# Kernel tuning notes

Measured on AMD Instinct MI355X. Metric: run time of the kernel, lower is better.

The kernel has to match this reference:

```python
import jax, jax.numpy as jnp
import numpy as np

N = 50000      # nodes
E = 1600000    # edges (avg degree 32)
D_IN = 128
HID = 64


def setup_inputs() -> dict:
    key = jax.random.key(0)
    ks = jax.random.split(key, 7)
    x = jax.random.normal(ks[0], (N, D_IN), dtype=jnp.float32)
    ei = jax.random.randint(ks[1], (2, E), 0, N, dtype=jnp.int32)
    ew = jax.random.uniform(ks[2], (E,), dtype=jnp.float32)
    # GCNConv linear weights (glorot-ish scale); lin has no bias, conv bias added post-aggregation
    W1 = jax.random.normal(ks[3], (HID, D_IN), dtype=jnp.float32) * (1.0 / np.sqrt(D_IN))
    b1 = jnp.zeros((HID,), dtype=jnp.float32)
    W2 = jax.random.normal(ks[4], (HID, HID), dtype=jnp.float32) * (1.0 / np.sqrt(HID))
    b2 = jnp.zeros((HID,), dtype=jnp.float32)
    return {"x": x, "ei": ei, "ew": ew, "W1": W1, "b1": b1, "W2": W2, "b2": b2}


def _gcn_conv(x, src, dst, ew_all, W, b, n_nodes):
    """PyG GCNConv: gcn_norm (self-loops already appended) + x@W.T, gather-scale-scatter, +b."""
    deg = jax.ops.segment_sum(ew_all, dst, num_segments=n_nodes)  # dst-side weighted degree
    dinv = jnp.where(deg > 0, jax.lax.rsqrt(deg), 0.0)            # deg^{-1/2}, inf->0
    norm = dinv[src] * ew_all * dinv[dst]                          # [E+N]
    h = x @ W.T                                                    # [N, hid]
    msg = h[src] * norm[:, None]                                   # gather + scale
    out = jax.ops.segment_sum(msg, dst, num_segments=n_nodes)     # scatter-add
    return out + b


def reference(x, ei, ew, W1, b1, W2, b2):
    n_nodes = x.shape[0]
    # add self loops once (fill value 1.0), shared by both conv layers
    loop = jnp.arange(n_nodes, dtype=ei.dtype)
    src = jnp.concatenate([ei[0], loop])
    dst = jnp.concatenate([ei[1], loop])
    ew_all = jnp.concatenate([ew, jnp.ones((n_nodes,), dtype=ew.dtype)])

    h1 = jax.nn.relu(_gcn_conv(x, src, dst, ew_all, W1, b1, n_nodes))
    # dropout is identity in eval mode
    h2 = _gcn_conv(h1, src, dst, ew_all, W2, b2, n_nodes)
    return h2 + h1
```

## Files before the change

kernel.cpp:

```cpp
#include <hip/hip_runtime.h>

#define HID 64
#define DIN 128
#define NBLK 512
#define CSH 14
#define CAP (1 << CSH)
#define PAD 68

typedef unsigned long long ull;
typedef unsigned short u16;

static __device__ __forceinline__ u16 f2bf(float f) {
  unsigned u = __float_as_uint(f);
  unsigned lsb = (u >> 16) & 1u;
  u += 0x7fffu + lsb;
  return (u16)(u >> 16);
}


template <int K, int NT, bool XT_PRELOADED>
__device__ __forceinline__ void gemm_tile(const float* __restrict__ X,
                                          const float* __restrict__ W,
                                          u16* __restrict__ out,
                                          float* XT, float* WL,
                                          int n0, int n_nodes, int tid) {
  constexpr int ROWS = NT / 8;
  const int tx = tid & 15;
  const int ty = tid >> 4;
  float acc[2][4] = {{0.f}};

  for (int ph = 0; ph < K / 64; ++ph) {
    const int d0 = ph * 64;
    __syncthreads();
    if (!XT_PRELOADED) {
#pragma unroll
      for (int k = 0; k < 2; ++k) {
        int f = tid + k * NT;
        int r = f >> 4, q = f & 15;
        int n = n0 + r;
        float4 xv = (n < n_nodes)
          ? *reinterpret_cast<const float4*>(&X[(size_t)n * K + d0 + 4 * q])
          : make_float4(0.f, 0.f, 0.f, 0.f);
        *reinterpret_cast<float4*>(&XT[r * PAD + 4 * q]) = xv;
      }
    }
#pragma unroll
    for (int k = 0; k < 1024 / NT; ++k) {
      int gq = tid + k * NT;
      int qd = gq >> 6, j = gq & 63;
      float4 wv = *reinterpret_cast<const float4*>(&W[(size_t)j * K + d0 + 4 * qd]);
      WL[(4 * qd + 0) * PAD + j] = wv.x;
      WL[(4 * qd + 1) * PAD + j] = wv.y;
      WL[(4 * qd + 2) * PAD + j] = wv.z;
      WL[(4 * qd + 3) * PAD + j] = wv.w;
    }
    __syncthreads();
#pragma unroll 4
    for (int dd = 0; dd < 64; dd += 4) {
      float4 ws[4];
#pragma unroll
      for (int dk = 0; dk < 4; ++dk)
        ws[dk] = *reinterpret_cast<const float4*>(&WL[(dd + dk) * PAD + 4 * tx]);
      float4 x0 = *reinterpret_cast<const float4*>(&XT[ty * PAD + dd]);
      float4 x1 = *reinterpret_cast<const float4*>(&XT[(ty + ROWS / 2) * PAD + dd]);
      float xm0[4] = {x0.x, x0.y, x0.z, x0.w};
      float xm1[4] = {x1.x, x1.y, x1.z, x1.w};
#pragma unroll
      for (int dk = 0; dk < 4; ++dk) {
        acc[0][0] = fmaf(xm0[dk], ws[dk].x, acc[0][0]);
        acc[0][1] = fmaf(xm0[dk], ws[dk].y, acc[0][1]);
        acc[0][2] = fmaf(xm0[dk], ws[dk].z, acc[0][2]);
        acc[0][3] = fmaf(xm0[dk], ws[dk].w, acc[0][3]);
        acc[1][0] = fmaf(xm1[dk], ws[dk].x, acc[1][0]);
        acc[1][1] = fmaf(xm1[dk], ws[dk].y, acc[1][1]);
        acc[1][2] = fmaf(xm1[dk], ws[dk].z, acc[1][2]);
        acc[1][3] = fmaf(xm1[dk], ws[dk].w, acc[1][3]);
      }
    }
  }

#pragma unroll
  for (int mi = 0; mi < 2; ++mi) {
    int n = n0 + mi * (ROWS / 2) + ty;
    if (n < n_nodes) {
      ushort4 o = make_ushort4(f2bf(acc[mi][0]), f2bf(acc[mi][1]),
                               f2bf(acc[mi][2]), f2bf(acc[mi][3]));
      *reinterpret_cast<ushort4*>(&out[(size_t)n * HID + 4 * tx]) = o;
    }
  }
}


__global__ __launch_bounds__(512) void k_build_gemm(const int* __restrict__ src,
                                                    const int* __restrict__ dst,
                                                    const float* __restrict__ ew,
                                                    int* __restrict__ cursor,
                                                    int2* __restrict__ bufA,
                                                    int E, int chunk,
                                                    const float* __restrict__ x,
                                                    const float* __restrict__ W1,
                                                    u16* __restrict__ h,
                                                    int n_nodes) {
  __shared__ float S[2 * 64 * PAD];
  int b = blockIdx.x, tid = threadIdx.x;
  if (b >= NBLK) {
    gemm_tile<DIN, 512, false>(x, W1, h, S, S + 64 * PAD, (b - NBLK) * 64, n_nodes, tid);
    return;
  }
  int* hst = (int*)S;
  int* cur = (int*)S + 256;
  if (tid < 256) hst[tid] = 0;
  __syncthreads();
  int e0 = b * chunk, e1 = min(E, e0 + chunk);
  int nfull = (e1 - e0) & ~3;
  int rtail = (e1 - e0) - nfull;
  for (int e = e0 + 4 * tid; e < e0 + nfull; e += 4 * 512) {
    int4 d4 = *reinterpret_cast<const int4*>(&dst[e]);
    atomicAdd(&hst[d4.x >> 8], 1);
    atomicAdd(&hst[d4.y >> 8], 1);
    atomicAdd(&hst[d4.z >> 8], 1);
    atomicAdd(&hst[d4.w >> 8], 1);
  }
  if (tid < rtail) atomicAdd(&hst[dst[e0 + nfull + tid] >> 8], 1);
  __syncthreads();
  if (tid < 256) {
    int c = hst[tid];
    int ofs = (c > 0) ? atomicAdd(&cursor[tid], c) : 0;
    cur[tid] = (tid << CSH) + ofs;
  }
  __syncthreads();
  for (int e = e0 + 4 * tid; e < e0 + nfull; e += 4 * 512) {
    int4 s4 = *reinterpret_cast<const int4*>(&src[e]);
    int4 d4 = *reinterpret_cast<const int4*>(&dst[e]);
    float4 w4 = *reinterpret_cast<const float4*>(&ew[e]);
    int p0 = atomicAdd(&cur[d4.x >> 8], 1);
    bufA[p0] = make_int2(__float_as_int(w4.x), (int)(((unsigned)s4.x << 16) | (unsigned)d4.x));
    int p1 = atomicAdd(&cur[d4.y >> 8], 1);
    bufA[p1] = make_int2(__float_as_int(w4.y), (int)(((unsigned)s4.y << 16) | (unsigned)d4.y));
    int p2 = atomicAdd(&cur[d4.z >> 8], 1);
    bufA[p2] = make_int2(__float_as_int(w4.z), (int)(((unsigned)s4.z << 16) | (unsigned)d4.z));
    int p3 = atomicAdd(&cur[d4.w >> 8], 1);
    bufA[p3] = make_int2(__float_as_int(w4.w), (int)(((unsigned)s4.w << 16) | (unsigned)d4.w));
  }
  if (tid < rtail) {
    int e = e0 + nfull + tid;
    int s = src[e], d = dst[e];
    int p = atomicAdd(&cur[d >> 8], 1);
    bufA[p] = make_int2(__float_as_int(ew[e]), (int)(((unsigned)s << 16) | (unsigned)d));
  }
}


__global__ __launch_bounds__(1024) void k_passB(const int2* __restrict__ bufA,
                                                const int* __restrict__ cursor,
                                                int2* __restrict__ bufB,
                                                int* __restrict__ offs,
                                                int* __restrict__ cnt,
                                                float* __restrict__ dinv,
                                                int NBC, int N) {
  int bin = blockIdx.x, tid = threadIdx.x;
  __shared__ int h2[256];
  __shared__ int cur[256];
  __shared__ float dg[256];
  int bbase = bin << CSH;
  int m = cursor[bin];
  if (tid < 256) { h2[tid] = 0; dg[tid] = 0.f; }
  __syncthreads();
  int2 rloc[16];
#pragma unroll
  for (int k = 0; k < 16; ++k) {
    int i = tid + k * 1024;
    if (i < m) {
      rloc[k] = bufA[bbase + i];
      atomicAdd(&h2[(unsigned)rloc[k].y & 255u], 1);
    }
  }
  __syncthreads();
  int own = (tid < 256) ? h2[tid] : 0;
  for (int o = 1; o < 256; o <<= 1) {
    int u = 0;
    if (tid < 256 && tid >= o) u = h2[tid - o];
    __syncthreads();
    if (tid < 256) h2[tid] += u;
    __syncthreads();
  }
  int nd = (bin << 8) + tid;
  if (tid < 256) {
    int excl = h2[tid] - own;
    cur[tid] = excl;
    if (nd < N) { offs[nd] = bbase + excl; cnt[nd] = own; }
  }
  __syncthreads();
#pragma unroll
  for (int k = 0; k < 16; ++k) {
    int i = tid + k * 1024;
    if (i < m) {
      int2 r = rloc[k];
      unsigned sd = (unsigned)r.y;
      int dl = (int)(sd & 255u);
      int p = atomicAdd(&cur[dl], 1);
      bufB[bbase + p] = make_int2(r.x, (int)(sd >> 16));
      atomicAdd(&dg[dl], __int_as_float(r.x));
    }
  }
  __syncthreads();
  if (tid < 256 && nd < N) dinv[nd] = rsqrtf(1.0f + dg[tid]);
}


__device__ __forceinline__ void bfma8(const uint4& v, float w, float* a) {
  a[0] = fmaf(__uint_as_float(v.x << 16), w, a[0]);
  a[1] = fmaf(__uint_as_float(v.x & 0xffff0000u), w, a[1]);
  a[2] = fmaf(__uint_as_float(v.y << 16), w, a[2]);
  a[3] = fmaf(__uint_as_float(v.y & 0xffff0000u), w, a[3]);
  a[4] = fmaf(__uint_as_float(v.z << 16), w, a[4]);
  a[5] = fmaf(__uint_as_float(v.z & 0xffff0000u), w, a[5]);
  a[6] = fmaf(__uint_as_float(v.w << 16), w, a[6]);
  a[7] = fmaf(__uint_as_float(v.w & 0xffff0000u), w, a[7]);
}

__device__ __forceinline__ void agg_node(const u16* __restrict__ h,
                                         const int2* __restrict__ recs,
                                         const float* __restrict__ dinv,
                                         int beg, int end, int node, float di,
                                         int lane, int p8, float* r) {
  float a[8], b[8];
  {
    uint4 v = *reinterpret_cast<const uint4*>(&h[(size_t)node * HID + p8]);
    a[0] = __uint_as_float(v.x << 16) * di;
    a[1] = __uint_as_float(v.x & 0xffff0000u) * di;
    a[2] = __uint_as_float(v.y << 16) * di;
    a[3] = __uint_as_float(v.y & 0xffff0000u) * di;
    a[4] = __uint_as_float(v.z << 16) * di;
    a[5] = __uint_as_float(v.z & 0xffff0000u) * di;
    a[6] = __uint_as_float(v.w << 16) * di;
    a[7] = __uint_as_float(v.w & 0xffff0000u) * di;
#pragma unroll
    for (int j = 0; j < 8; ++j) b[j] = 0.f;
  }

  const int gb = lane & 56;
  const int l7 = lane & 7;
  int i = beg;
  if (i + 8 <= end) {
    ull rr = *reinterpret_cast<const ull*>(&recs[i + l7]);
    float dv = dinv[(int)(rr >> 32)];
    for (;;) {
      float wd = __uint_as_float((unsigned)rr) * dv;
      ull ru = (rr & 0xffffffff00000000ull) | (ull)__float_as_uint(wd);
      bool more = (i + 16 <= end);
      ull rr_n = 0; float dv_n = 0.f;
      if (more) {
        rr_n = *reinterpret_cast<const ull*>(&recs[i + 8 + l7]);
        dv_n = dinv[(int)(rr_n >> 32)];
      }
#pragma unroll
      for (int k = 0; k < 8; ++k) {
        ull q = __shfl(ru, gb | k, 64);
        float wk = __uint_as_float((unsigned)q);
        int sk = (int)(q >> 32);
        uint4 vk = *reinterpret_cast<const uint4*>(&h[(size_t)sk * HID + p8]);
        bfma8(vk, wk, (k & 1) ? b : a);
      }
      i += 8;
      if (!more) break;
      rr = rr_n; dv = dv_n;
    }
  }
  if (i + 4 <= end) {
    int2 r0 = recs[i];     int2 r1 = recs[i + 1];
    int2 r2 = recs[i + 2]; int2 r3 = recs[i + 3];
    uint4 v0 = *reinterpret_cast<const uint4*>(&h[(size_t)r0.y * HID + p8]);
    uint4 v1 = *reinterpret_cast<const uint4*>(&h[(size_t)r1.y * HID + p8]);
    uint4 v2 = *reinterpret_cast<const uint4*>(&h[(size_t)r2.y * HID + p8]);
    uint4 v3 = *reinterpret_cast<const uint4*>(&h[(size_t)r3.y * HID + p8]);
    bfma8(v0, __int_as_float(r0.x) * dinv[r0.y], a);
    bfma8(v1, __int_as_float(r1.x) * dinv[r1.y], b);
    bfma8(v2, __int_as_float(r2.x) * dinv[r2.y], a);
    bfma8(v3, __int_as_float(r3.x) * dinv[r3.y], b);
    i += 4;
  }
  if (i + 2 <= end) {
    int2 r0 = recs[i];     int2 r1 = recs[i + 1];
    uint4 v0 = *reinterpret_cast<const uint4*>(&h[(size_t)r0.y * HID + p8]);
    uint4 v1 = *reinterpret_cast<const uint4*>(&h[(size_t)r1.y * HID + p8]);
    bfma8(v0, __int_as_float(r0.x) * dinv[r0.y], a);
    bfma8(v1, __int_as_float(r1.x) * dinv[r1.y], b);
    i += 2;
  }
  if (i < end) {
    int2 r0 = recs[i];
    uint4 v0 = *reinterpret_cast<const uint4*>(&h[(size_t)r0.y * HID + p8]);
    bfma8(v0, __int_as_float(r0.x) * dinv[r0.y], a);
  }
#pragma unroll
  for (int j = 0; j < 8; ++j) r[j] = (a[j] + b[j]) * di;
}


__global__ __launch_bounds__(256) void k_agg_gemm(const u16* __restrict__ h,
                                                  const int2* __restrict__ recs,
                                                  const int* __restrict__ offs,
                                                  const int* __restrict__ cnt,
                                                  const float* __restrict__ dinv,
                                                  const float* __restrict__ bias,
                                                  const float* __restrict__ W2,
                                                  float* __restrict__ h1,
                                                  u16* __restrict__ h2,
                                                  int n_nodes) {
  __shared__ float S[(32 + 64) * PAD];
  float* XT = S;
  float* WL = S + 32 * PAD;
  int tid = threadIdx.x;
  int lane = tid & 63;
  int p8 = (lane & 7) * 8;
  int nl = (tid >> 6) * 8 + (lane >> 3);
  int node = blockIdx.x * 32 + nl;
  if (node < n_nodes) {
    float di = dinv[node];
    float r[8];
    agg_node(h, recs, dinv, offs[node], offs[node] + cnt[node], node, di,
             lane, p8, r);
    float4 bb0 = *reinterpret_cast<const float4*>(&bias[p8]);
    float4 bb1 = *reinterpret_cast<const float4*>(&bias[p8 + 4]);
    r[0] += bb0.x; r[1] += bb0.y; r[2] += bb0.z; r[3] += bb0.w;
    r[4] += bb1.x; r[5] += bb1.y; r[6] += bb1.z; r[7] += bb1.w;
#pragma unroll
    for (int j = 0; j < 8; ++j) r[j] = fmaxf(r[j], 0.f);
    float4 lo = make_float4(r[0], r[1], r[2], r[3]);
    float4 hi = make_float4(r[4], r[5], r[6], r[7]);
    *reinterpret_cast<float4*>(&h1[(size_t)node * HID + p8]) = lo;
    *reinterpret_cast<float4*>(&h1[(size_t)node * HID + p8 + 4]) = hi;
    *reinterpret_cast<float4*>(&XT[nl * PAD + p8]) = lo;
    *reinterpret_cast<float4*>(&XT[nl * PAD + p8 + 4]) = hi;
  }
  gemm_tile<HID, 256, true>(nullptr, W2, h2, XT, WL, blockIdx.x * 32, n_nodes, tid);
}


__global__ __launch_bounds__(256) void k_agg2(const u16* __restrict__ h,
                                              const int2* __restrict__ recs,
                                              const int* __restrict__ offs,
                                              const int* __restrict__ cnt,
                                              const float* __restrict__ dinv,
                                              const float* __restrict__ bias,
                                              const float* __restrict__ resid,
                                              float* __restrict__ out, int n_nodes) {
  int tid = threadIdx.x;
  int lane = tid & 63;
  int p8 = (lane & 7) * 8;
  int node = (blockIdx.x * 4 + (tid >> 6)) * 8 + (lane >> 3);
  if (node >= n_nodes) return;
  float di = dinv[node];
  float r[8];
  agg_node(h, recs, dinv, offs[node], offs[node] + cnt[node], node, di,
           lane, p8, r);
  float4 bb0 = *reinterpret_cast<const float4*>(&bias[p8]);
  float4 bb1 = *reinterpret_cast<const float4*>(&bias[p8 + 4]);
  float4 rs0 = *reinterpret_cast<const float4*>(&resid[(size_t)node * HID + p8]);
  float4 rs1 = *reinterpret_cast<const float4*>(&resid[(size_t)node * HID + p8 + 4]);
  r[0] += bb0.x + rs0.x; r[1] += bb0.y + rs0.y;
  r[2] += bb0.z + rs0.z; r[3] += bb0.w + rs0.w;
  r[4] += bb1.x + rs1.x; r[5] += bb1.y + rs1.y;
  r[6] += bb1.z + rs1.z; r[7] += bb1.w + rs1.w;
  *reinterpret_cast<float4*>(&out[(size_t)node * HID + p8]) =
      make_float4(r[0], r[1], r[2], r[3]);
  *reinterpret_cast<float4*>(&out[(size_t)node * HID + p8 + 4]) =
      make_float4(r[4], r[5], r[6], r[7]);
}


extern "C" void kernel_launch(void* const* d_in, const int* in_sizes, int n_in,
                              void* d_out, int out_size, void* d_ws, size_t ws_size,
                              hipStream_t stream) {
  const float* x  = (const float*)d_in[0];
  const int*   ei = (const int*)d_in[1];
  const float* ew = (const float*)d_in[2];
  const float* W1 = (const float*)d_in[3];
  const float* b1 = (const float*)d_in[4];
  const float* W2 = (const float*)d_in[5];
  const float* b2 = (const float*)d_in[6];
  float* out = (float*)d_out;

  const int N = in_sizes[0] / DIN;
  const int E = in_sizes[2];
  const int* src = ei;
  const int* dst = ei + E;

  const int NBC = (N + 255) >> 8;
  const int chunk = (((E + NBLK - 1) / NBLK) + 3) & ~3;
  const int nslab = NBC << CSH;

  char* p = (char*)d_ws;
  auto carve = [&](size_t bytes) {
    char* r = p;
    p += (bytes + 255) & ~(size_t)255;
    return r;
  };
  int*   cursor = (int*)carve(256 * 4);
  int*   offs   = (int*)carve((size_t)N * 4);
  int*   cnt    = (int*)carve((size_t)N * 4);
  float* dinv   = (float*)carve((size_t)N * 4);
  int2*  bufA   = (int2*)carve((size_t)nslab * 8);
  int2*  bufB   = (int2*)carve((size_t)nslab * 8);
  u16*   h      = (u16*)carve((size_t)N * HID * 2);
  u16*   h2     = (u16*)carve((size_t)N * HID * 2);
  float* h1     = (float*)carve((size_t)N * HID * 4);

  int gblk  = (N + 63) / 64;
  int gblk2 = (N + 31) / 32;
  int ablk  = (N + 31) / 32;

  hipMemsetAsync(cursor, 0, 256 * 4, stream);
  k_build_gemm<<<NBLK + gblk, 512, 0, stream>>>(src, dst, ew, cursor, bufA, E, chunk,
                                                x, W1, h, N);
  k_passB<<<NBC, 1024, 0, stream>>>(bufA, cursor, bufB, offs, cnt, dinv, NBC, N);
  k_agg_gemm<<<gblk2, 256, 0, stream>>>(h, bufB, offs, cnt, dinv, b1, W2, h1, h2, N);
  k_agg2<<<ablk, 256, 0, stream>>>(h2, bufB, offs, cnt, dinv, b2, h1, out, N);
}
```

Before: 209.5 us.

## Split bin histogram per half-block and keep first edge loads in registers

The edge-binning phase now keeps two shared-memory histograms and cursor arrays, one per 256-thread half of the block, to reduce contention on the LDS atomics. The src, dst and weight values for each thread's first two int4 groups are held in registers between the count pass and the scatter pass, so they are not read from global memory twice. Only edges beyond the first 4096 in a chunk are re-read. Scalar tail handling was removed, so correctness now depends on chunk boundaries being multiples of 4.

```diff
diff --git a/kernel.cpp b/kernel.cpp
--- a/kernel.cpp
+++ b/kernel.cpp
@@ -107,46 +107,77 @@
     gemm_tile<DIN, 512, false>(x, W1, h, S, S + 64 * PAD, (b - NBLK) * 64, n_nodes, tid);
     return;
   }
-  int* hst = (int*)S;
-  int* cur = (int*)S + 256;
-  if (tid < 256) hst[tid] = 0;
+  int* h0   = (int*)S;
+  int* h1_  = (int*)S + 256;
+  int* cur0 = (int*)S + 512;
+  int* cur1 = (int*)S + 768;
+  if (tid < 256) { h0[tid] = 0; h1_[tid] = 0; }
   __syncthreads();
   int e0 = b * chunk, e1 = min(E, e0 + chunk);
-  int nfull = (e1 - e0) & ~3;
-  int rtail = (e1 - e0) - nfull;
-  for (int e = e0 + 4 * tid; e < e0 + nfull; e += 4 * 512) {
-    int4 d4 = *reinterpret_cast<const int4*>(&dst[e]);
-    atomicAdd(&hst[d4.x >> 8], 1);
-    atomicAdd(&hst[d4.y >> 8], 1);
-    atomicAdd(&hst[d4.z >> 8], 1);
-    atomicAdd(&hst[d4.w >> 8], 1);
-  }
-  if (tid < rtail) atomicAdd(&hst[dst[e0 + nfull + tid] >> 8], 1);
+  const int half = tid >> 8;
+  int* hh = half ? h1_ : h0;
+  int4 s4[2], d4[2];
+  float4 w4[2];
+  bool val[2];
+#pragma unroll
+  for (int it = 0; it < 2; ++it) {
+    int e = e0 + 4 * tid + it * 2048;
+    val[it] = (e < e1);
+    if (val[it]) {
+      s4[it] = *reinterpret_cast<const int4*>(&src[e]);
+      d4[it] = *reinterpret_cast<const int4*>(&dst[e]);
+      w4[it] = *reinterpret_cast<const float4*>(&ew[e]);
+      atomicAdd(&hh[d4[it].x >> 8], 1);
+      atomicAdd(&hh[d4[it].y >> 8], 1);
+      atomicAdd(&hh[d4[it].z >> 8], 1);
+      atomicAdd(&hh[d4[it].w >> 8], 1);
+    }
+  }
+  for (int e = e0 + 4096 + 4 * tid; e < e1; e += 2048) {
+    int4 dd = *reinterpret_cast<const int4*>(&dst[e]);
+    atomicAdd(&hh[dd.x >> 8], 1);
+    atomicAdd(&hh[dd.y >> 8], 1);
+    atomicAdd(&hh[dd.z >> 8], 1);
+    atomicAdd(&hh[dd.w >> 8], 1);
+  }
   __syncthreads();
   if (tid < 256) {
-    int c = hst[tid];
-    int ofs = (c > 0) ? atomicAdd(&cursor[tid], c) : 0;
-    cur[tid] = (tid << CSH) + ofs;
-  }
-  __syncthreads();
-  for (int e = e0 + 4 * tid; e < e0 + nfull; e += 4 * 512) {
-    int4 s4 = *reinterpret_cast<const int4*>(&src[e]);
-    int4 d4 = *reinterpret_cast<const int4*>(&dst[e]);
-    float4 w4 = *reinterpret_cast<const float4*>(&ew[e]);
-    int p0 = atomicAdd(&cur[d4.x >> 8], 1);
-    bufA[p0] = make_int2(__float_as_int(w4.x), (int)(((unsigned)s4.x << 16) | (unsigned)d4.x));
-    int p1 = atomicAdd(&cur[d4.y >> 8], 1);
-    bufA[p1] = make_int2(__float_as_int(w4.y), (int)(((unsigned)s4.y << 16) | (unsigned)d4.y));
-    int p2 = atomicAdd(&cur[d4.z >> 8], 1);
-    bufA[p2] = make_int2(__float_as_int(w4.z), (int)(((unsigned)s4.z << 16) | (unsigned)d4.z));
-    int p3 = atomicAdd(&cur[d4.w >> 8], 1);
-    bufA[p3] = make_int2(__float_as_int(w4.w), (int)(((unsigned)s4.w << 16) | (unsigned)d4.w));
-  }
-  if (tid < rtail) {
-    int e = e0 + nfull + tid;
-    int s = src[e], d = dst[e];
-    int p = atomicAdd(&cur[d >> 8], 1);
-    bufA[p] = make_int2(__float_as_int(ew[e]), (int)(((unsigned)s << 16) | (unsigned)d));
+    int c0 = h0[tid], c1 = h1_[tid], tot = c0 + c1;
+    int ofs = (tot > 0) ? atomicAdd(&cursor[tid], tot) : 0;
+    cur0[tid] = (tid << CSH) + ofs;
+    cur1[tid] = (tid << CSH) + ofs + c0;
+  }
+  __syncthreads();
+  int* cc = half ? cur1 : cur0;
+#pragma unroll
+  for (int it = 0; it < 2; ++it) {
+    if (val[it]) {
+      int p0 = atomicAdd(&cc[d4[it].x >> 8], 1);
+      bufA[p0] = make_int2(__float_as_int(w4[it].x),
+                           (int)(((unsigned)s4[it].x << 16) | (unsigned)d4[it].x));
+      int p1 = atomicAdd(&cc[d4[it].y >> 8], 1);
+      bufA[p1] = make_int2(__float_as_int(w4[it].y),
+                           (int)(((unsigned)s4[it].y << 16) | (unsigned)d4[it].y));
+      int p2 = atomicAdd(&cc[d4[it].z >> 8], 1);
+      bufA[p2] = make_int2(__float_as_int(w4[it].z),
+                           (int)(((unsigned)s4[it].z << 16) | (unsigned)d4[it].z));
+      int p3 = atomicAdd(&cc[d4[it].w >> 8], 1);
+      bufA[p3] = make_int2(__float_as_int(w4[it].w),
+                           (int)(((unsigned)s4[it].w << 16) | (unsigned)d4[it].w));
+    }
+  }
+  for (int e = e0 + 4096 + 4 * tid; e < e1; e += 2048) {
+    int4 ss = *reinterpret_cast<const int4*>(&src[e]);
+    int4 dd = *reinterpret_cast<const int4*>(&dst[e]);
+    float4 ww = *reinterpret_cast<const float4*>(&ew[e]);
+    int p0 = atomicAdd(&cc[dd.x >> 8], 1);
+    bufA[p0] = make_int2(__float_as_int(ww.x), (int)(((unsigned)ss.x << 16) | (unsigned)dd.x));
+    int p1 = atomicAdd(&cc[dd.y >> 8], 1);
+    bufA[p1] = make_int2(__float_as_int(ww.y), (int)(((unsigned)ss.y << 16) | (unsigned)dd.y));
+    int p2 = atomicAdd(&cc[dd.z >> 8], 1);
+    bufA[p2] = make_int2(__float_as_int(ww.z), (int)(((unsigned)ss.z << 16) | (unsigned)dd.z));
+    int p3 = atomicAdd(&cc[dd.w >> 8], 1);
+    bufA[p3] = make_int2(__float_as_int(ww.w), (int)(((unsigned)ss.w << 16) | (unsigned)dd.w));
   }
 }
 
```

After: 209.9 us. About the same (+0.2%).
